# Kernel tuning notes

Measured on AMD Instinct MI355X. Metric: run time of the kernel, lower is better.

## Reference

```python
import jax, jax.numpy as jnp
import numpy as np

HIDDEN = 64
SEQ_LEN = 96
NUM_BASIS = 10
NUM_CLASSES = 2
IN_SIZE = 1
B = 16384


def _basis(x, W, a, c):
    # x: (B, in); a, c: (in, K); W: (in, out, K)
    # KAN-style ferroelectric basis: sum_{i,k} W[i,o,k] * tanh(a[i,k]*x[b,i] + c[i,k])
    phi = jnp.tanh(x[:, :, None] * a[None] + c[None])  # (B, in, K)
    return jnp.einsum('bik,iok->bo', phi, W)           # (B, out)


def setup_inputs() -> dict:
    key = jax.random.key(0)
    ks = jax.random.split(key, 11)
    s_in = 1.0 / np.sqrt(IN_SIZE * NUM_BASIS)
    s_h = 1.0 / np.sqrt(HIDDEN * NUM_BASIS)
    return {
        'x': jax.random.normal(ks[0], (B, SEQ_LEN), dtype=jnp.float32),
        'Wx': jax.random.normal(ks[1], (IN_SIZE, HIDDEN, NUM_BASIS), dtype=jnp.float32) * s_in,
        'ax': jax.random.normal(ks[2], (IN_SIZE, NUM_BASIS), dtype=jnp.float32),
        'cx': jax.random.normal(ks[3], (IN_SIZE, NUM_BASIS), dtype=jnp.float32),
        'Wh': jax.random.normal(ks[4], (HIDDEN, HIDDEN, NUM_BASIS), dtype=jnp.float32) * s_h,
        'ah': jax.random.normal(ks[5], (HIDDEN, NUM_BASIS), dtype=jnp.float32),
        'ch': jax.random.normal(ks[6], (HIDDEN, NUM_BASIS), dtype=jnp.float32),
        'Wc': jax.random.normal(ks[7], (HIDDEN, HIDDEN, NUM_BASIS), dtype=jnp.float32) * s_h,
        'ac': jax.random.normal(ks[8], (HIDDEN, NUM_BASIS), dtype=jnp.float32),
        'cc': jax.random.normal(ks[9], (HIDDEN, NUM_BASIS), dtype=jnp.float32),
        'Wout': jax.random.normal(ks[10], (HIDDEN, NUM_CLASSES), dtype=jnp.float32),
    }


def reference(x, Wx, ax, cx, Wh, ah, ch, Wc, ac, cc, Wout):
    Bsz = x.shape[0]

    def step(h, x_t):
        # x_t: (B,) -> (B, 1)
        x_phi = _basis(x_t[:, None], Wx, ax, cx)   # (B, HIDDEN)
        h_phi = _basis(h, Wh, ah, ch)              # (B, HIDDEN)
        comb = jnp.tanh(jnp.concatenate([x_phi, h_phi], axis=1))  # (B, 2H)
        return comb[:, :HIDDEN], None

    h0 = jnp.zeros((Bsz, HIDDEN), dtype=x.dtype)
    h, _ = jax.lax.scan(step, h0, jnp.transpose(x))  # scan over SEQ_LEN

    # KAN classifier head
    phi = jnp.tanh(_basis(h, Wc, ac, cc))  # (B, HIDDEN)
    return phi @ Wout                      # (B, NUM_CLASSES)
```

## Files before the change

kernel.cpp:

```cpp
#include <hip/hip_runtime.h>

#define HIDDEN 64
#define SEQLEN 96
#define NB 10
#define BATCH 16384
#define NCLASS 2
#define KTOT (HIDDEN * NB)
#define NKC (KTOT / 32)
#define MT 32
#define NW 4
#define KCW (NKC / NW)
#define HSS 33
#define CRS 66

typedef __attribute__((ext_vector_type(8))) short bf16x8;
typedef __attribute__((ext_vector_type(4))) float f32x4;

__device__ __forceinline__ float fast_tanh(float x) {
    float e = __expf(x + x);
    float r = __builtin_amdgcn_rcpf(e + 1.0f);
    return fmaf(-2.0f, r, 1.0f);
}

__device__ __forceinline__ unsigned bf16_rn(float f) {
    unsigned u = __float_as_uint(f);
    return (u + 0x8000u) >> 16;
}

__global__ __launch_bounds__(256) void prep_wb(const float* __restrict__ Wc,
                                               ushort* __restrict__ Wp) {
    int e = blockIdx.x * 256 + threadIdx.x;
    int j = e & 7;
    int lane = (e >> 3) & 63;
    int rest = e >> 9;
    int nt = rest & 3;
    int kcg = rest >> 2;
    int q = kcg * 32 + (lane >> 4) * 8 + j;
    int o = nt * 16 + (lane & 15);
    int i = q / 10;
    int k = q - i * 10;
    Wp[e] = (ushort)bf16_rn(Wc[i * (HIDDEN * NB) + o * NB + k]);
}

__global__ __launch_bounds__(256, 4) void kan_mfma(
    const float* __restrict__ x,
    const float* __restrict__ Wx,
    const float* __restrict__ ax, const float* __restrict__ cx,
    const float* __restrict__ ac,
    const float* __restrict__ cc,
    const float* __restrict__ Wout,
    const ushort* __restrict__ Wp,
    float* __restrict__ out)
{
    __shared__ float hs[65 * HSS];
    __shared__ float Cred[MT * CRS];
    __shared__ float outb[MT * NCLASS];

    const int lane = threadIdx.x;
    const int w    = threadIdx.y;
    const int tid  = w * 64 + lane;
    const int bb   = blockIdx.x * MT;

    for (int idx = tid; idx < MT * CRS; idx += 256) Cred[idx] = 0.0f;

    {
        const int sm = tid & 31;
        const int sg = tid >> 5;
        const float u = x[(bb + sm) * SEQLEN + (SEQLEN - 1)];
        float t[NB];
#pragma unroll
        for (int k = 0; k < NB; ++k)
            t[k] = fast_tanh(fmaf(ax[k], u, cx[k]));
#pragma unroll
        for (int r = 0; r < 8; ++r) {
            const int i = sg * 8 + r;
            const float* wxr = Wx + i * NB;
            float hx = 0.0f;
#pragma unroll
            for (int k = 0; k < NB; ++k)
                hx = fmaf(wxr[k], t[k], hx);
            hs[i * HSS + sm] = fast_tanh(hx);
        }
    }
    __syncthreads();

    const int m    = lane & 15;
    const int quad = lane >> 4;
    f32x4 a00 = {0,0,0,0}, a01 = {0,0,0,0}, a02 = {0,0,0,0}, a03 = {0,0,0,0};
    f32x4 a10 = {0,0,0,0}, a11 = {0,0,0,0}, a12 = {0,0,0,0}, a13 = {0,0,0,0};

#pragma unroll
    for (int c = 0; c < KCW; ++c) {
        const int kcg = w * KCW + c;
        const int q0  = kcg * 32 + quad * 8;
        const int i0  = q0 / 10;
        const int r0  = q0 - i0 * 10;
        const float h0a = hs[i0 * HSS + m];
        const float h1a = hs[(i0 + 1) * HSS + m];
        const float h0b = hs[i0 * HSS + 16 + m];
        const float h1b = hs[(i0 + 1) * HSS + 16 + m];
        const float4 av0 = *(const float4*)(ac + q0);
        const float4 av1 = *(const float4*)(ac + q0 + 4);
        const float4 cv0 = *(const float4*)(cc + q0);
        const float4 cv1 = *(const float4*)(cc + q0 + 4);
        const float av[8] = {av0.x,av0.y,av0.z,av0.w,av1.x,av1.y,av1.z,av1.w};
        const float cv[8] = {cv0.x,cv0.y,cv0.z,cv0.w,cv1.x,cv1.y,cv1.z,cv1.w};

        union { unsigned u[4]; bf16x8 v; } af0, af1;
#pragma unroll
        for (int jj = 0; jj < 4; ++jj) {
            const int j0 = 2 * jj, j1 = 2 * jj + 1;
            const float hA0 = (r0 + j0 >= 10) ? h1a : h0a;
            const float hA1 = (r0 + j1 >= 10) ? h1a : h0a;
            const float hB0 = (r0 + j0 >= 10) ? h1b : h0b;
            const float hB1 = (r0 + j1 >= 10) ? h1b : h0b;
            const float pA0 = fast_tanh(fmaf(av[j0], hA0, cv[j0]));
            const float pA1 = fast_tanh(fmaf(av[j1], hA1, cv[j1]));
            const float pB0 = fast_tanh(fmaf(av[j0], hB0, cv[j0]));
            const float pB1 = fast_tanh(fmaf(av[j1], hB1, cv[j1]));
            af0.u[jj] = bf16_rn(pA0) | (bf16_rn(pA1) << 16);
            af1.u[jj] = bf16_rn(pB0) | (bf16_rn(pB1) << 16);
        }

        const ushort* wb = Wp + (size_t)(kcg * 4) * 512 + lane * 8;
        const bf16x8 b0 = *(const bf16x8*)(wb);
        const bf16x8 b1 = *(const bf16x8*)(wb + 512);
        const bf16x8 b2 = *(const bf16x8*)(wb + 1024);
        const bf16x8 b3 = *(const bf16x8*)(wb + 1536);
        a00 = __builtin_amdgcn_mfma_f32_16x16x32_bf16(af0.v, b0, a00, 0, 0, 0);
        a01 = __builtin_amdgcn_mfma_f32_16x16x32_bf16(af0.v, b1, a01, 0, 0, 0);
        a02 = __builtin_amdgcn_mfma_f32_16x16x32_bf16(af0.v, b2, a02, 0, 0, 0);
        a03 = __builtin_amdgcn_mfma_f32_16x16x32_bf16(af0.v, b3, a03, 0, 0, 0);
        a10 = __builtin_amdgcn_mfma_f32_16x16x32_bf16(af1.v, b0, a10, 0, 0, 0);
        a11 = __builtin_amdgcn_mfma_f32_16x16x32_bf16(af1.v, b1, a11, 0, 0, 0);
        a12 = __builtin_amdgcn_mfma_f32_16x16x32_bf16(af1.v, b2, a12, 0, 0, 0);
        a13 = __builtin_amdgcn_mfma_f32_16x16x32_bf16(af1.v, b3, a13, 0, 0, 0);
    }

#pragma unroll
    for (int reg = 0; reg < 4; ++reg) {
        const int row = quad * 4 + reg;
        atomicAdd(&Cred[(row)      * CRS +  0 + m], a00[reg]);
        atomicAdd(&Cred[(row)      * CRS + 16 + m], a01[reg]);
        atomicAdd(&Cred[(row)      * CRS + 32 + m], a02[reg]);
        atomicAdd(&Cred[(row)      * CRS + 48 + m], a03[reg]);
        atomicAdd(&Cred[(row + 16) * CRS +  0 + m], a10[reg]);
        atomicAdd(&Cred[(row + 16) * CRS + 16 + m], a11[reg]);
        atomicAdd(&Cred[(row + 16) * CRS + 32 + m], a12[reg]);
        atomicAdd(&Cred[(row + 16) * CRS + 48 + m], a13[reg]);
    }
    __syncthreads();

    {
        const int mm = tid >> 3;
        const int ob = (tid & 7) * 8;
        float r0 = 0.0f, r1 = 0.0f;
#pragma unroll
        for (int t2 = 0; t2 < 8; ++t2) {
            const int o = ob + t2;
            const float g = fast_tanh(Cred[mm * CRS + o]);
            r0 = fmaf(g, Wout[o * NCLASS + 0], r0);
            r1 = fmaf(g, Wout[o * NCLASS + 1], r1);
        }
#pragma unroll
        for (int off = 4; off > 0; off >>= 1) {
            r0 += __shfl_down(r0, off, 8);
            r1 += __shfl_down(r1, off, 8);
        }
        if ((tid & 7) == 0) {
            outb[mm * NCLASS + 0] = r0;
            outb[mm * NCLASS + 1] = r1;
        }
    }
    __syncthreads();
    if (tid < MT * NCLASS)
        out[bb * NCLASS + tid] = outb[tid];

}

extern "C" void kernel_launch(void* const* d_in, const int* in_sizes, int n_in,
                              void* d_out, int out_size, void* d_ws, size_t ws_size,
                              hipStream_t stream) {
    const float* x    = (const float*)d_in[0];
    const float* Wx   = (const float*)d_in[1];
    const float* ax   = (const float*)d_in[2];
    const float* cx   = (const float*)d_in[3];
    const float* Wc   = (const float*)d_in[7];
    const float* ac   = (const float*)d_in[8];
    const float* cc   = (const float*)d_in[9];
    const float* Wout = (const float*)d_in[10];
    float* out  = (float*)d_out;
    ushort* Wp  = (ushort*)d_ws;

    prep_wb<<<dim3(NKC * 4 * 512 / 256), dim3(256), 0, stream>>>(Wc, Wp);
    kan_mfma<<<dim3(BATCH / MT), dim3(64, NW), 0, stream>>>(
        x, Wx, ax, cx, ac, cc, Wout, Wp, out);
}
```

Baseline: 102.7 us.

## Fuse weight repack into main kernel via per-block LDS repack in two halves

Drops the separate prep kernel and has every block convert and repack the classifier weights from fp32 into bf16 MFMA layout in shared memory, one output half at a time. Basis activations are kept in registers so the second half of outputs can reuse them after the repack. The aim is to remove a kernel launch and the global round-trip of the packed weights. In exchange every block now redoes the full weight conversion, adds extra barriers, and carries more register pressure, with occupancy hint lowered to 2.

```diff
diff --git a/kernel.cpp b/kernel.cpp
--- a/kernel.cpp
+++ b/kernel.cpp
@@ -27,31 +27,48 @@
     return (u + 0x8000u) >> 16;
 }
 
-__global__ __launch_bounds__(256) void prep_wb(const float* __restrict__ Wc,
-                                               ushort* __restrict__ Wp) {
-    int e = blockIdx.x * 256 + threadIdx.x;
-    int j = e & 7;
-    int lane = (e >> 3) & 63;
-    int rest = e >> 9;
-    int nt = rest & 3;
-    int kcg = rest >> 2;
-    int q = kcg * 32 + (lane >> 4) * 8 + j;
-    int o = nt * 16 + (lane & 15);
-    int i = q / 10;
-    int k = q - i * 10;
-    Wp[e] = (ushort)bf16_rn(Wc[i * (HIDDEN * NB) + o * NB + k]);
-}
-
-__global__ __launch_bounds__(256, 4) void kan_mfma(
+__device__ __forceinline__ void repack_half(const float* __restrict__ Wc,
+                                            ushort* Wp_lds, int tid, int half) {
+    const int i    = tid >> 2;
+    const int part = tid & 3;
+    const float* src = Wc + i * (HIDDEN * NB) + half * (32 * NB) + part * 80;
+    unsigned* Wp32 = (unsigned*)Wp_lds;
+#pragma unroll
+    for (int hp = 0; hp < 2; ++hp) {
+        float fv[40];
+#pragma unroll
+        for (int v = 0; v < 10; ++v)
+            *(float4*)(fv + 4 * v) = *(const float4*)(src + hp * 40 + 4 * v);
+#pragma unroll
+        for (int ro = 0; ro < 4; ++ro) {
+            const int oo  = part * 8 + hp * 4 + ro;
+            const int ntl = oo >> 4, n = oo & 15;
+#pragma unroll
+            for (int kk = 0; kk < 5; ++kk) {
+                const int k   = 2 * kk;
+                const int q   = i * NB + k;
+                const int kcg = q >> 5;
+                const int lhi = (q >> 3) & 3;
+                const int j   = q & 7;
+                const unsigned val = bf16_rn(fv[ro * 10 + k]) |
+                                     (bf16_rn(fv[ro * 10 + k + 1]) << 16);
+                Wp32[((((kcg * 2 + ntl) * 64) + lhi * 16 + n) * 8 + j) >> 1] = val;
+            }
+        }
+    }
+}
+
+__global__ __launch_bounds__(256, 2) void kan_one(
     const float* __restrict__ x,
     const float* __restrict__ Wx,
     const float* __restrict__ ax, const float* __restrict__ cx,
+    const float* __restrict__ Wc,
     const float* __restrict__ ac,
     const float* __restrict__ cc,
     const float* __restrict__ Wout,
-    const ushort* __restrict__ Wp,
     float* __restrict__ out)
 {
+    __shared__ ushort Wp[NKC * 2 * 64 * 8];
     __shared__ float hs[65 * HSS];
     __shared__ float Cred[MT * CRS];
     __shared__ float outb[MT * NCLASS];
@@ -63,6 +80,7 @@
 
     for (int idx = tid; idx < MT * CRS; idx += 256) Cred[idx] = 0.0f;
 
+    repack_half(Wc, Wp, tid, 0);
     {
         const int sm = tid & 31;
         const int sg = tid >> 5;
@@ -86,8 +104,9 @@
 
     const int m    = lane & 15;
     const int quad = lane >> 4;
-    f32x4 a00 = {0,0,0,0}, a01 = {0,0,0,0}, a02 = {0,0,0,0}, a03 = {0,0,0,0};
-    f32x4 a10 = {0,0,0,0}, a11 = {0,0,0,0}, a12 = {0,0,0,0}, a13 = {0,0,0,0};
+    bf16x8 afs0[KCW], afs1[KCW];
+    f32x4 A00 = {0,0,0,0}, A01 = {0,0,0,0}, A10 = {0,0,0,0}, A11 = {0,0,0,0};
+    f32x4 B00 = {0,0,0,0}, B01 = {0,0,0,0}, B10 = {0,0,0,0}, B11 = {0,0,0,0};
 
 #pragma unroll
     for (int c = 0; c < KCW; ++c) {
@@ -121,33 +140,45 @@
             af0.u[jj] = bf16_rn(pA0) | (bf16_rn(pA1) << 16);
             af1.u[jj] = bf16_rn(pB0) | (bf16_rn(pB1) << 16);
         }
-
-        const ushort* wb = Wp + (size_t)(kcg * 4) * 512 + lane * 8;
+        afs0[c] = af0.v;
+        afs1[c] = af1.v;
+
+        const ushort* wb = Wp + (size_t)(kcg * 2) * 512 + lane * 8;
         const bf16x8 b0 = *(const bf16x8*)(wb);
         const bf16x8 b1 = *(const bf16x8*)(wb + 512);
-        const bf16x8 b2 = *(const bf16x8*)(wb + 1024);
-        const bf16x8 b3 = *(const bf16x8*)(wb + 1536);
-        a00 = __builtin_amdgcn_mfma_f32_16x16x32_bf16(af0.v, b0, a00, 0, 0, 0);
-        a01 = __builtin_amdgcn_mfma_f32_16x16x32_bf16(af0.v, b1, a01, 0, 0, 0);
-        a02 = __builtin_amdgcn_mfma_f32_16x16x32_bf16(af0.v, b2, a02, 0, 0, 0);
-        a03 = __builtin_amdgcn_mfma_f32_16x16x32_bf16(af0.v, b3, a03, 0, 0, 0);
-        a10 = __builtin_amdgcn_mfma_f32_16x16x32_bf16(af1.v, b0, a10, 0, 0, 0);
-        a11 = __builtin_amdgcn_mfma_f32_16x16x32_bf16(af1.v, b1, a11, 0, 0, 0);
-        a12 = __builtin_amdgcn_mfma_f32_16x16x32_bf16(af1.v, b2, a12, 0, 0, 0);
-        a13 = __builtin_amdgcn_mfma_f32_16x16x32_bf16(af1.v, b3, a13, 0, 0, 0);
+        A00 = __builtin_amdgcn_mfma_f32_16x16x32_bf16(af0.v, b0, A00, 0, 0, 0);
+        A01 = __builtin_amdgcn_mfma_f32_16x16x32_bf16(af0.v, b1, A01, 0, 0, 0);
+        A10 = __builtin_amdgcn_mfma_f32_16x16x32_bf16(af1.v, b0, A10, 0, 0, 0);
+        A11 = __builtin_amdgcn_mfma_f32_16x16x32_bf16(af1.v, b1, A11, 0, 0, 0);
+    }
+    __syncthreads();
+
+    repack_half(Wc, Wp, tid, 1);
+    __syncthreads();
+
+#pragma unroll
+    for (int c = 0; c < KCW; ++c) {
+        const int kcg = w * KCW + c;
+        const ushort* wb = Wp + (size_t)(kcg * 2) * 512 + lane * 8;
+        const bf16x8 b0 = *(const bf16x8*)(wb);
+        const bf16x8 b1 = *(const bf16x8*)(wb + 512);
+        B00 = __builtin_amdgcn_mfma_f32_16x16x32_bf16(afs0[c], b0, B00, 0, 0, 0);
+        B01 = __builtin_amdgcn_mfma_f32_16x16x32_bf16(afs0[c], b1, B01, 0, 0, 0);
+        B10 = __builtin_amdgcn_mfma_f32_16x16x32_bf16(afs1[c], b0, B10, 0, 0, 0);
+        B11 = __builtin_amdgcn_mfma_f32_16x16x32_bf16(afs1[c], b1, B11, 0, 0, 0);
     }
 
 #pragma unroll
     for (int reg = 0; reg < 4; ++reg) {
         const int row = quad * 4 + reg;
-        atomicAdd(&Cred[(row)      * CRS +  0 + m], a00[reg]);
-        atomicAdd(&Cred[(row)      * CRS + 16 + m], a01[reg]);
-        atomicAdd(&Cred[(row)      * CRS + 32 + m], a02[reg]);
-        atomicAdd(&Cred[(row)      * CRS + 48 + m], a03[reg]);
-        atomicAdd(&Cred[(row + 16) * CRS +  0 + m], a10[reg]);
-        atomicAdd(&Cred[(row + 16) * CRS + 16 + m], a11[reg]);
-        atomicAdd(&Cred[(row + 16) * CRS + 32 + m], a12[reg]);
-        atomicAdd(&Cred[(row + 16) * CRS + 48 + m], a13[reg]);
+        atomicAdd(&Cred[(row)      * CRS +  0 + m], A00[reg]);
+        atomicAdd(&Cred[(row)      * CRS + 16 + m], A01[reg]);
+        atomicAdd(&Cred[(row + 16) * CRS +  0 + m], A10[reg]);
+        atomicAdd(&Cred[(row + 16) * CRS + 16 + m], A11[reg]);
+        atomicAdd(&Cred[(row)      * CRS + 32 + m], B00[reg]);
+        atomicAdd(&Cred[(row)      * CRS + 48 + m], B01[reg]);
+        atomicAdd(&Cred[(row + 16) * CRS + 32 + m], B10[reg]);
+        atomicAdd(&Cred[(row + 16) * CRS + 48 + m], B11[reg]);
     }
     __syncthreads();
 
@@ -175,7 +206,6 @@
     __syncthreads();
     if (tid < MT * NCLASS)
         out[bb * NCLASS + tid] = outb[tid];
-
 }
 
 extern "C" void kernel_launch(void* const* d_in, const int* in_sizes, int n_in,
@@ -189,10 +219,8 @@
     const float* ac   = (const float*)d_in[8];
     const float* cc   = (const float*)d_in[9];
     const float* Wout = (const float*)d_in[10];
-    float* out  = (float*)d_out;
-    ushort* Wp  = (ushort*)d_ws;
-
-    prep_wb<<<dim3(NKC * 4 * 512 / 256), dim3(256), 0, stream>>>(Wc, Wp);
-    kan_mfma<<<dim3(BATCH / MT), dim3(64, NW), 0, stream>>>(
-        x, Wx, ax, cx, ac, cc, Wout, Wp, out);
-}
+    float* out = (float*)d_out;
+
+    kan_one<<<dim3(BATCH / MT), dim3(64, NW), 0, stream>>>(
+        x, Wx, ax, cx, Wc, ac, cc, Wout, out);
+}
```

Measured after the change: 108.6 us. 1.06x slower.
